# Performance work log

Measured on AMD Instinct MI355X. Metric: run time of the kernel, lower is better.

Reference implementation:

```python
import jax, jax.numpy as jnp
import numpy as np

FEAT = 512   # PLIP backbone dim
HID = 256
N_CLS_HEADS = 11   # each 3 classes -> 33 logits
N_REG_HEADS = 55   # each 1 output

def _xavier(key, shape):
    fan_in, fan_out = shape[0], shape[1]
    limit = float(np.sqrt(6.0 / (fan_in + fan_out)))
    return jax.random.uniform(key, shape, jnp.float32, -limit, limit)

def setup_inputs() -> dict:
    key = jax.random.key(0)
    ks = jax.random.split(key, 8)
    N = 200000
    x = jax.random.normal(ks[0], (1, N, FEAT), jnp.float32)
    return {
        'x': x,
        'W1': _xavier(ks[1], (FEAT, HID)), 'b1': jnp.zeros((HID,), jnp.float32),
        'Wa': _xavier(ks[2], (HID, HID)), 'ba': jnp.zeros((HID,), jnp.float32),
        'Wb': _xavier(ks[3], (HID, HID)), 'bb': jnp.zeros((HID,), jnp.float32),
        'Wc': _xavier(ks[4], (HID, 1)),  'bc': jnp.zeros((1,), jnp.float32),
        'Wr': _xavier(ks[5], (HID, HID)), 'br': jnp.zeros((HID,), jnp.float32),
        # 11 classifier heads (3 classes each) stacked into one [256, 33] GEMM
        'Wcls': _xavier(ks[6], (HID, 3 * N_CLS_HEADS)), 'bcls': jnp.zeros((3 * N_CLS_HEADS,), jnp.float32),
        'Wreg': _xavier(ks[7], (HID, N_REG_HEADS)), 'breg': jnp.zeros((N_REG_HEADS,), jnp.float32),
    }

def reference(x, W1, b1, Wa, ba, Wb, bb, Wc, bc, Wr, br, Wcls, bcls, Wreg, breg):
    xp = x[0]                                   # [N, 512]
    h = jax.nn.relu(xp @ W1 + b1)               # [N, 256]  (dropout inactive at eval)
    a = jnp.tanh(h @ Wa + ba)                   # [N, 256]
    b = jax.nn.sigmoid(h @ Wb + bb)             # [N, 256]
    A_raw = ((a * b) @ Wc + bc).T               # [1, N]
    A = jax.nn.softmax(A_raw, axis=1)           # [1, N]
    global_feat = A @ h                         # [1, 256]
    hr = jax.nn.relu(global_feat @ Wr + br)     # [1, 256]
    cls_logits = hr @ Wcls + bcls               # [1, 33] = 11 heads x 3 classes
    reg_values = (hr @ Wreg + breg)[0]          # [55]   (per-head squeeze(1))
    return A, global_feat, cls_logits, reg_values
```

## Files before the change

### kernel.cpp

```cpp
#include <hip/hip_runtime.h>
#include <stdint.h>

#define FEAT 512
#define HID  256
#define TILE 64
#define G1   768

typedef __attribute__((ext_vector_type(8))) short   short8;
typedef __attribute__((ext_vector_type(4))) float   floatx4;

__device__ inline unsigned short f2bf(float x){
  union { float f; uint32_t u; } v; v.f = x;
  uint32_t u = v.u;
  u += 0x7FFFu + ((u >> 16) & 1u);
  return (unsigned short)(u >> 16);
}
__device__ inline float bf2f(unsigned short h){
  union { uint32_t u; float f; } v; v.u = ((uint32_t)h) << 16;
  return v.f;
}
__device__ inline float sigm_f(float x){ return 1.f/(1.f + __expf(-x)); }
__device__ inline float tanh_f(float x){ return 2.f/(1.f + __expf(-2.f*x)) - 1.f; }

__global__ void prep_weights(const float* __restrict__ W1, const float* __restrict__ Wa,
                             const float* __restrict__ Wb,
                             unsigned short* __restrict__ W1bf,
                             unsigned short* __restrict__ Wabf,
                             unsigned short* __restrict__ Wbbf){
  int t = blockIdx.x*256 + threadIdx.x;
  const float* src; unsigned short* dst; int g;
  if      (t < 16384){ src = W1; dst = W1bf; g = t; }
  else if (t < 24576){ src = Wa; dst = Wabf; g = t - 16384; }
  else if (t < 32768){ src = Wb; dst = Wbbf; g = t - 24576; }
  else return;
  int lane = g & 63, nt = (g >> 6) & 15, kb = g >> 10;
  int col  = nt*16 + (lane & 15);
  int row0 = kb*32 + (lane >> 4)*8;
  unsigned short* d = dst + (size_t)g*8;
  const float*    s = src + (size_t)row0*HID + col;
  #pragma unroll
  for (int j = 0; j < 8; ++j) d[j] = f2bf(s[(size_t)j*HID]);
}

__global__ __launch_bounds__(256, 3) void fused_main(
    const float* __restrict__ x,
    const float* __restrict__ b1, const float* __restrict__ ba,
    const float* __restrict__ bb, const float* __restrict__ Wc,
    const float* __restrict__ bc,
    const unsigned short* __restrict__ W1bf,
    const unsigned short* __restrict__ Wabf,
    const unsigned short* __restrict__ Wbbf,
    float* __restrict__ s_buf, float* __restrict__ partials, int ntiles)
{
  __shared__ alignas(16) unsigned short Hs[64][264];
  __shared__ alignas(16) unsigned short Ws[8192];
  __shared__ float pbuf[4][16];

  const int tid  = threadIdx.x;
  const int wave = tid >> 6, lane = tid & 63;
  const int quad = lane >> 4, l15 = lane & 15;

  float m_run = -INFINITY, l_run = 0.f;
  float g0 = 0.f, g1 = 0.f, g2 = 0.f, g3 = 0.f;
  const float bcv = bc[0];

  for (int t = blockIdx.x; t < ntiles; t += gridDim.x){
    const int tokw = t*TILE + wave*16;

    floatx4 acc[16];
    #pragma unroll
    for (int nt = 0; nt < 16; ++nt){
      float bv = b1[nt*16 + l15];
      floatx4 tmp = {bv, bv, bv, bv};
      acc[nt] = tmp;
    }
    const float* xrow = x + (size_t)(tokw + l15)*FEAT + quad*8;
    #pragma unroll 1
    for (int kb = 0; kb < 16; ++kb){
      __syncthreads();
      { const short8* srcv = (const short8*)(W1bf + (size_t)kb*8192);
        short8* dstv = (short8*)Ws;
        #pragma unroll
        for (int c = 0; c < 4; ++c) dstv[tid + 256*c] = srcv[tid + 256*c]; }
      __syncthreads();
      const float* xp = xrow + kb*32;
      float4 xa = *(const float4*)xp;
      float4 xb = *(const float4*)(xp + 4);
      union { short8 v; unsigned short u[8]; } af;
      af.u[0]=f2bf(xa.x); af.u[1]=f2bf(xa.y); af.u[2]=f2bf(xa.z); af.u[3]=f2bf(xa.w);
      af.u[4]=f2bf(xb.x); af.u[5]=f2bf(xb.y); af.u[6]=f2bf(xb.z); af.u[7]=f2bf(xb.w);
      #pragma unroll
      for (int nt = 0; nt < 16; ++nt){
        short8 bfv = *(const short8*)&Ws[nt*512 + lane*8];
        acc[nt] = __builtin_amdgcn_mfma_f32_16x16x32_bf16(af.v, bfv, acc[nt], 0, 0, 0);
      }
    }
    #pragma unroll
    for (int nt = 0; nt < 16; ++nt){
      #pragma unroll
      for (int r = 0; r < 4; ++r){
        float hv = fmaxf(acc[nt][r], 0.f);
        Hs[wave*16 + quad*4 + r][nt*16 + l15] = f2bf(hv);
      }
    }

    float sp0 = 0.f, sp1 = 0.f, sp2 = 0.f, sp3 = 0.f;
    #pragma unroll 1
    for (int nh = 0; nh < 2; ++nh){
      floatx4 aacc[8], bacc[8];
      #pragma unroll
      for (int nt = 0; nt < 8; ++nt){
        int col = (nh*8 + nt)*16 + l15;
        float av = ba[col], bv = bb[col];
        floatx4 ta = {av, av, av, av}; aacc[nt] = ta;
        floatx4 tb = {bv, bv, bv, bv}; bacc[nt] = tb;
      }
      #pragma unroll 1
      for (int kb = 0; kb < 8; ++kb){
        __syncthreads();
        { const short8* sA = (const short8*)(Wabf + (size_t)(kb*16 + nh*8)*512);
          const short8* sB = (const short8*)(Wbbf + (size_t)(kb*16 + nh*8)*512);
          short8* dstv = (short8*)Ws;
          dstv[tid]       = sA[tid];
          dstv[tid + 256] = sA[tid + 256];
          dstv[tid + 512] = sB[tid];
          dstv[tid + 768] = sB[tid + 256]; }
        __syncthreads();
        short8 af = *(const short8*)&Hs[wave*16 + l15][kb*32 + quad*8];
        #pragma unroll
        for (int nt = 0; nt < 8; ++nt){
          short8 bA = *(const short8*)&Ws[nt*512 + lane*8];
          short8 bB = *(const short8*)&Ws[4096 + nt*512 + lane*8];
          aacc[nt] = __builtin_amdgcn_mfma_f32_16x16x32_bf16(af, bA, aacc[nt], 0, 0, 0);
          bacc[nt] = __builtin_amdgcn_mfma_f32_16x16x32_bf16(af, bB, bacc[nt], 0, 0, 0);
        }
      }
      #pragma unroll
      for (int nt = 0; nt < 8; ++nt){
        int col = (nh*8 + nt)*16 + l15;
        float wcv = Wc[col];
        sp0 += tanh_f(aacc[nt][0]) * sigm_f(bacc[nt][0]) * wcv;
        sp1 += tanh_f(aacc[nt][1]) * sigm_f(bacc[nt][1]) * wcv;
        sp2 += tanh_f(aacc[nt][2]) * sigm_f(bacc[nt][2]) * wcv;
        sp3 += tanh_f(aacc[nt][3]) * sigm_f(bacc[nt][3]) * wcv;
      }
    }
    #pragma unroll
    for (int mk = 1; mk < 16; mk <<= 1){
      sp0 += __shfl_xor(sp0, mk, 64);
      sp1 += __shfl_xor(sp1, mk, 64);
      sp2 += __shfl_xor(sp2, mk, 64);
      sp3 += __shfl_xor(sp3, mk, 64);
    }
    float s0 = sp0 + bcv, s1 = sp1 + bcv, s2 = sp2 + bcv, s3 = sp3 + bcv;
    if (l15 == 0){
      float* sb = s_buf + tokw + quad*4;
      sb[0] = s0; sb[1] = s1; sb[2] = s2; sb[3] = s3;
    }
    float tmax = fmaxf(fmaxf(s0, s1), fmaxf(s2, s3));
    tmax = fmaxf(tmax, __shfl_xor(tmax, 16, 64));
    tmax = fmaxf(tmax, __shfl_xor(tmax, 32, 64));
    float m_new = fmaxf(m_run, tmax);
    float alpha = __expf(m_run - m_new);
    float p0 = __expf(s0 - m_new), p1 = __expf(s1 - m_new);
    float p2 = __expf(s2 - m_new), p3 = __expf(s3 - m_new);
    float psum = p0 + p1 + p2 + p3;
    psum += __shfl_xor(psum, 16, 64);
    psum += __shfl_xor(psum, 32, 64);
    l_run = l_run*alpha + psum;
    m_run = m_new;
    if (l15 == 0){
      pbuf[wave][quad*4+0] = p0; pbuf[wave][quad*4+1] = p1;
      pbuf[wave][quad*4+2] = p2; pbuf[wave][quad*4+3] = p3;
    }
    g0 *= alpha; g1 *= alpha; g2 *= alpha; g3 *= alpha;
    #pragma unroll
    for (int rw = 0; rw < 16; ++rw){
      float pr = pbuf[wave][rw];
      const unsigned short* hp = &Hs[wave*16 + rw][lane*4];
      g0 += pr*bf2f(hp[0]); g1 += pr*bf2f(hp[1]);
      g2 += pr*bf2f(hp[2]); g3 += pr*bf2f(hp[3]);
    }
  }

  __syncthreads();
  float* fred = (float*)Ws;
  if (lane == 0) fred[wave] = m_run;
  __syncthreads();
  float M = fmaxf(fmaxf(fred[0], fred[1]), fmaxf(fred[2], fred[3]));
  float sc = (m_run == -INFINITY) ? 0.f : __expf(m_run - M);
  if (lane == 0) fred[4 + wave] = l_run * sc;
  fred[8 + wave*256 + lane*4 + 0] = g0*sc;
  fred[8 + wave*256 + lane*4 + 1] = g1*sc;
  fred[8 + wave*256 + lane*4 + 2] = g2*sc;
  fred[8 + wave*256 + lane*4 + 3] = g3*sc;
  __syncthreads();
  float gsum = fred[8 + 0*256 + tid] + fred[8 + 1*256 + tid]
             + fred[8 + 2*256 + tid] + fred[8 + 3*256 + tid];
  float* P = partials + (size_t)blockIdx.x*258;
  if (tid == 0){ P[0] = M; P[1] = fred[4] + fred[5] + fred[6] + fred[7]; }
  P[2 + tid] = gsum;
}

__global__ void reduce_heads(const float* __restrict__ partials,
    const float* __restrict__ Wr,   const float* __restrict__ br,
    const float* __restrict__ Wcls, const float* __restrict__ bcls,
    const float* __restrict__ Wreg, const float* __restrict__ breg,
    float* __restrict__ out, float* __restrict__ ML, int ntok)
{
  __shared__ float red[256];
  __shared__ float scw[G1];
  __shared__ float gf[256];
  __shared__ float hr[256];
  int t = threadIdx.x;

  float lm = -INFINITY;
  for (int i = t; i < G1; i += 256) lm = fmaxf(lm, partials[(size_t)i*258]);
  red[t] = lm; __syncthreads();
  for (int s = 128; s > 0; s >>= 1){ if (t < s) red[t] = fmaxf(red[t], red[t+s]); __syncthreads(); }
  float M = red[0];
  __syncthreads();

  float ll = 0.f;
  for (int i = t; i < G1; i += 256){
    float w = __expf(partials[(size_t)i*258] - M);
    scw[i] = w;
    ll += partials[(size_t)i*258 + 1] * w;
  }
  red[t] = ll; __syncthreads();
  for (int s = 128; s > 0; s >>= 1){ if (t < s) red[t] += red[t+s]; __syncthreads(); }
  float L = red[0];

  float g = 0.f;
  for (int i = 0; i < G1; ++i) g += partials[(size_t)i*258 + 2 + t] * scw[i];
  float gfv = g / L;
  gf[t] = gfv;
  out[ntok + t] = gfv;
  if (t == 0){ ML[0] = M; ML[1] = 1.f / L; }
  __syncthreads();

  float h = br[t];
  for (int c = 0; c < 256; ++c) h += gf[c] * Wr[c*256 + t];
  h = fmaxf(h, 0.f);
  hr[t] = h; __syncthreads();

  if (t < 33){
    float v = bcls[t];
    for (int j = 0; j < 256; ++j) v += hr[j] * Wcls[j*33 + t];
    out[ntok + 256 + t] = v;
  }
  if (t < 55){
    float v = breg[t];
    for (int j = 0; j < 256; ++j) v += hr[j] * Wreg[j*55 + t];
    out[ntok + 289 + t] = v;
  }
}

__global__ void finalize_A(const float* __restrict__ s_buf, const float* __restrict__ ML,
                           float* __restrict__ out, int ntok){
  int i = blockIdx.x*256 + threadIdx.x;
  if (i < ntok) out[i] = __expf(s_buf[i] - ML[0]) * ML[1];
}

extern "C" void kernel_launch(void* const* d_in, const int* in_sizes, int n_in,
                              void* d_out, int out_size, void* d_ws, size_t ws_size,
                              hipStream_t stream){
  (void)n_in; (void)out_size; (void)ws_size;
  const float* x    = (const float*)d_in[0];
  const float* W1   = (const float*)d_in[1];
  const float* b1   = (const float*)d_in[2];
  const float* Wa   = (const float*)d_in[3];
  const float* ba   = (const float*)d_in[4];
  const float* Wb   = (const float*)d_in[5];
  const float* bb   = (const float*)d_in[6];
  const float* Wc   = (const float*)d_in[7];
  const float* bc   = (const float*)d_in[8];
  const float* Wr   = (const float*)d_in[9];
  const float* br   = (const float*)d_in[10];
  const float* Wcls = (const float*)d_in[11];
  const float* bcls = (const float*)d_in[12];
  const float* Wreg = (const float*)d_in[13];
  const float* breg = (const float*)d_in[14];
  float* out = (float*)d_out;

  const int ntok   = in_sizes[0] / FEAT;
  const int ntiles = ntok / TILE;

  char* ws = (char*)d_ws;
  float* s_buf = (float*)ws;
  size_t off = (size_t)ntok * 4;
  float* partials = (float*)(ws + off); off += (size_t)G1*258*4;
  float* ML = (float*)(ws + off); off += 16;
  unsigned short* W1bf = (unsigned short*)(ws + off); off += (size_t)FEAT*HID*2;
  unsigned short* Wabf = (unsigned short*)(ws + off); off += (size_t)HID*HID*2;
  unsigned short* Wbbf = (unsigned short*)(ws + off); off += (size_t)HID*HID*2;

  prep_weights<<<128, 256, 0, stream>>>(W1, Wa, Wb, W1bf, Wabf, Wbbf);
  fused_main<<<G1, 256, 0, stream>>>(x, b1, ba, bb, Wc, bc, W1bf, Wabf, Wbbf,
                                     s_buf, partials, ntiles);
  reduce_heads<<<1, 256, 0, stream>>>(partials, Wr, br, Wcls, bcls, Wreg, breg,
                                      out, ML, ntok);
  finalize_A<<<(ntok + 255)/256, 256, 0, stream>>>(s_buf, ML, out, ntok);
}
```

Measured before the change: 750.2 us.

## Double-buffer weight tiles via direct global-to-LDS loads and prefetch activations

```diff
diff --git a/kernel.cpp b/kernel.cpp
--- a/kernel.cpp
+++ b/kernel.cpp
@@ -4,10 +4,18 @@
 #define FEAT 512
 #define HID  256
 #define TILE 64
-#define G1   768
+#define PART 512
+#define S1   64
 
 typedef __attribute__((ext_vector_type(8))) short   short8;
 typedef __attribute__((ext_vector_type(4))) float   floatx4;
+typedef unsigned int u32;
+#define AS1 __attribute__((address_space(1)))
+#define AS3 __attribute__((address_space(3)))
+
+__device__ inline void gl_lds16(const void* g, void* l){
+  __builtin_amdgcn_global_load_lds((const AS1 u32*)g, (AS3 u32*)l, 16, 0, 0);
+}
 
 __device__ inline unsigned short f2bf(float x){
   union { float f; uint32_t u; } v; v.f = x;
@@ -23,77 +31,101 @@
 __device__ inline float tanh_f(float x){ return 2.f/(1.f + __expf(-2.f*x)) - 1.f; }
 
 __global__ void prep_weights(const float* __restrict__ W1, const float* __restrict__ Wa,
-                             const float* __restrict__ Wb,
-                             unsigned short* __restrict__ W1bf,
-                             unsigned short* __restrict__ Wabf,
-                             unsigned short* __restrict__ Wbbf){
+                             const float* __restrict__ Wb, unsigned short* __restrict__ blob){
   int t = blockIdx.x*256 + threadIdx.x;
-  const float* src; unsigned short* dst; int g;
-  if      (t < 16384){ src = W1; dst = W1bf; g = t; }
-  else if (t < 24576){ src = Wa; dst = Wabf; g = t - 16384; }
-  else if (t < 32768){ src = Wb; dst = Wbbf; g = t - 24576; }
-  else return;
-  int lane = g & 63, nt = (g >> 6) & 15, kb = g >> 10;
-  int col  = nt*16 + (lane & 15);
-  int row0 = kb*32 + (lane >> 4)*8;
-  unsigned short* d = dst + (size_t)g*8;
-  const float*    s = src + (size_t)row0*HID + col;
-  #pragma unroll
-  for (int j = 0; j < 8; ++j) d[j] = f2bf(s[(size_t)j*HID]);
-}
-
-__global__ __launch_bounds__(256, 3) void fused_main(
+  if (t >= 32768) return;
+  int r = t >> 10, s = t & 1023;
+  int lane = s & 63, l15 = lane & 15, quad = lane >> 4;
+  const float* src; int col, row0;
+  if (r < 16){
+    int nt = s >> 6;
+    src = W1; col = nt*16 + l15; row0 = r*32 + quad*8;
+  } else {
+    int r2 = r - 16, nh = r2 >> 3, kb = r2 & 7;
+    int half = s >> 9, nt2 = (s >> 6) & 7;
+    src = half ? Wb : Wa;
+    col = (nh*8 + nt2)*16 + l15; row0 = kb*32 + quad*8;
+  }
+  unsigned short* d = blob + (size_t)t*8;
+  const float*   sp = src + (size_t)row0*HID + col;
+  #pragma unroll
+  for (int j = 0; j < 8; ++j) d[j] = f2bf(sp[(size_t)j*HID]);
+}
+
+__global__ __launch_bounds__(256, 2) void fused_main(
     const float* __restrict__ x,
     const float* __restrict__ b1, const float* __restrict__ ba,
     const float* __restrict__ bb, const float* __restrict__ Wc,
     const float* __restrict__ bc,
-    const unsigned short* __restrict__ W1bf,
-    const unsigned short* __restrict__ Wabf,
-    const unsigned short* __restrict__ Wbbf,
+    const unsigned short* __restrict__ blob,
     float* __restrict__ s_buf, float* __restrict__ partials, int ntiles)
 {
   __shared__ alignas(16) unsigned short Hs[64][264];
-  __shared__ alignas(16) unsigned short Ws[8192];
+  __shared__ alignas(16) unsigned short Ws[2][8192];
   __shared__ float pbuf[4][16];
 
   const int tid  = threadIdx.x;
   const int wave = tid >> 6, lane = tid & 63;
   const int quad = lane >> 4, l15 = lane & 15;
 
+  auto stage = [&](int rnd, int buf){
+    #pragma unroll
+    for (int c = 0; c < 4; ++c){
+      const unsigned short* gp = blob + (size_t)rnd*8192 + (wave*4 + c)*512 + lane*8;
+      gl_lds16((const void*)gp, (void*)&Ws[buf][(wave*4 + c)*512]);
+    }
+  };
+
+  float b1r[16], bar[16], bbr[16], wcr[16];
+  #pragma unroll
+  for (int i = 0; i < 16; ++i){
+    int ci = i*16 + l15;
+    b1r[i] = b1[ci]; bar[i] = ba[ci]; bbr[i] = bb[ci]; wcr[i] = Wc[ci];
+  }
+  const float bcv = bc[0];
+
   float m_run = -INFINITY, l_run = 0.f;
   float g0 = 0.f, g1 = 0.f, g2 = 0.f, g3 = 0.f;
-  const float bcv = bc[0];
-
+
+  float4 xa = {0,0,0,0}, xb = {0,0,0,0};
+  if (blockIdx.x < ntiles){
+    const float* xr = x + (size_t)(blockIdx.x*TILE + wave*16 + l15)*FEAT + quad*8;
+    xa = *(const float4*)xr; xb = *(const float4*)(xr + 4);
+  }
+  stage(0, 0);
+  __syncthreads();
+
+  #pragma unroll 1
   for (int t = blockIdx.x; t < ntiles; t += gridDim.x){
     const int tokw = t*TILE + wave*16;
+    const float* xrow = x + (size_t)(tokw + l15)*FEAT + quad*8;
 
     floatx4 acc[16];
     #pragma unroll
     for (int nt = 0; nt < 16; ++nt){
-      float bv = b1[nt*16 + l15];
+      float bv = b1r[nt];
       floatx4 tmp = {bv, bv, bv, bv};
       acc[nt] = tmp;
     }
-    const float* xrow = x + (size_t)(tokw + l15)*FEAT + quad*8;
-    #pragma unroll 1
+    #pragma unroll 2
     for (int kb = 0; kb < 16; ++kb){
-      __syncthreads();
-      { const short8* srcv = (const short8*)(W1bf + (size_t)kb*8192);
-        short8* dstv = (short8*)Ws;
-        #pragma unroll
-        for (int c = 0; c < 4; ++c) dstv[tid + 256*c] = srcv[tid + 256*c]; }
-      __syncthreads();
-      const float* xp = xrow + kb*32;
-      float4 xa = *(const float4*)xp;
-      float4 xb = *(const float4*)(xp + 4);
+      stage(kb + 1, (kb + 1) & 1);
+      float4 xa_n, xb_n;
+      if (kb < 15){
+        const float* xp = xrow + (kb + 1)*32;
+        xa_n = *(const float4*)xp; xb_n = *(const float4*)(xp + 4);
+      }
       union { short8 v; unsigned short u[8]; } af;
       af.u[0]=f2bf(xa.x); af.u[1]=f2bf(xa.y); af.u[2]=f2bf(xa.z); af.u[3]=f2bf(xa.w);
       af.u[4]=f2bf(xb.x); af.u[5]=f2bf(xb.y); af.u[6]=f2bf(xb.z); af.u[7]=f2bf(xb.w);
+      const unsigned short* wsb = Ws[kb & 1];
       #pragma unroll
       for (int nt = 0; nt < 16; ++nt){
-        short8 bfv = *(const short8*)&Ws[nt*512 + lane*8];
+        short8 bfv = *(const short8*)&wsb[nt*512 + lane*8];
         acc[nt] = __builtin_amdgcn_mfma_f32_16x16x32_bf16(af.v, bfv, acc[nt], 0, 0, 0);
       }
+      __syncthreads();
+      if (kb < 15){ xa = xa_n; xb = xb_n; }
     }
     #pragma unroll
     for (int nt = 0; nt < 16; ++nt){
@@ -104,45 +136,46 @@
       }
     }
 
+    {
+      int tn = t + gridDim.x;
+      if (tn < ntiles){
+        const float* xr = x + (size_t)(tn*TILE + wave*16 + l15)*FEAT + quad*8;
+        xa = *(const float4*)xr; xb = *(const float4*)(xr + 4);
+      }
+    }
+
     float sp0 = 0.f, sp1 = 0.f, sp2 = 0.f, sp3 = 0.f;
-    #pragma unroll 1
+    #pragma unroll
     for (int nh = 0; nh < 2; ++nh){
       floatx4 aacc[8], bacc[8];
       #pragma unroll
-      for (int nt = 0; nt < 8; ++nt){
-        int col = (nh*8 + nt)*16 + l15;
-        float av = ba[col], bv = bb[col];
-        floatx4 ta = {av, av, av, av}; aacc[nt] = ta;
-        floatx4 tb = {bv, bv, bv, bv}; bacc[nt] = tb;
-      }
-      #pragma unroll 1
+      for (int nt2 = 0; nt2 < 8; ++nt2){
+        float av = bar[nh*8 + nt2], bv = bbr[nh*8 + nt2];
+        floatx4 ta = {av, av, av, av}; aacc[nt2] = ta;
+        floatx4 tb = {bv, bv, bv, bv}; bacc[nt2] = tb;
+      }
+      #pragma unroll 2
       for (int kb = 0; kb < 8; ++kb){
+        const int r = nh*8 + kb;
+        stage((r == 15) ? 0 : (17 + r), (r + 1) & 1);
+        short8 af2 = *(const short8*)&Hs[wave*16 + l15][kb*32 + quad*8];
+        const unsigned short* wsb = Ws[r & 1];
+        #pragma unroll
+        for (int nt2 = 0; nt2 < 8; ++nt2){
+          short8 bA = *(const short8*)&wsb[nt2*512 + lane*8];
+          short8 bB = *(const short8*)&wsb[4096 + nt2*512 + lane*8];
+          aacc[nt2] = __builtin_amdgcn_mfma_f32_16x16x32_bf16(af2, bA, aacc[nt2], 0, 0, 0);
+          bacc[nt2] = __builtin_amdgcn_mfma_f32_16x16x32_bf16(af2, bB, bacc[nt2], 0, 0, 0);
+        }
         __syncthreads();
-        { const short8* sA = (const short8*)(Wabf + (size_t)(kb*16 + nh*8)*512);
-          const short8* sB = (const short8*)(Wbbf + (size_t)(kb*16 + nh*8)*512);
-          short8* dstv = (short8*)Ws;
-          dstv[tid]       = sA[tid];
-          dstv[tid + 256] = sA[tid + 256];
-          dstv[tid + 512] = sB[tid];
-          dstv[tid + 768] = sB[tid + 256]; }
-        __syncthreads();
-        short8 af = *(const short8*)&Hs[wave*16 + l15][kb*32 + quad*8];
-        #pragma unroll
-        for (int nt = 0; nt < 8; ++nt){
-          short8 bA = *(const short8*)&Ws[nt*512 + lane*8];
-          short8 bB = *(const short8*)&Ws[4096 + nt*512 + lane*8];
-          aacc[nt] = __builtin_amdgcn_mfma_f32_16x16x32_bf16(af, bA, aacc[nt], 0, 0, 0);
-          bacc[nt] = __builtin_amdgcn_mfma_f32_16x16x32_bf16(af, bB, bacc[nt], 0, 0, 0);
-        }
       }
       #pragma unroll
-      for (int nt = 0; nt < 8; ++nt){
-        int col = (nh*8 + nt)*16 + l15;
-        float wcv = Wc[col];
-        sp0 += tanh_f(aacc[nt][0]) * sigm_f(bacc[nt][0]) * wcv;
-        sp1 += tanh_f(aacc[nt][1]) * sigm_f(bacc[nt][1]) * wcv;
-        sp2 += tanh_f(aacc[nt][2]) * sigm_f(bacc[nt][2]) * wcv;
-        sp3 += tanh_f(aacc[nt][3]) * sigm_f(bacc[nt][3]) * wcv;
+      for (int nt2 = 0; nt2 < 8; ++nt2){
+        float wcv = wcr[nh*8 + nt2];
+        sp0 += tanh_f(aacc[nt2][0]) * sigm_f(bacc[nt2][0]) * wcv;
+        sp1 += tanh_f(aacc[nt2][1]) * sigm_f(bacc[nt2][1]) * wcv;
+        sp2 += tanh_f(aacc[nt2][2]) * sigm_f(bacc[nt2][2]) * wcv;
+        sp3 += tanh_f(aacc[nt2][3]) * sigm_f(bacc[nt2][3]) * wcv;
       }
     }
     #pragma unroll
@@ -184,7 +217,7 @@
   }
 
   __syncthreads();
-  float* fred = (float*)Ws;
+  float* fred = (float*)(&Ws[0][0]);
   if (lane == 0) fred[wave] = m_run;
   __syncthreads();
   float M = fmaxf(fmaxf(fred[0], fred[1]), fmaxf(fred[2], fred[3]));
@@ -202,37 +235,58 @@
   P[2 + tid] = gsum;
 }
 
-__global__ void reduce_heads(const float* __restrict__ partials,
+__global__ void reduce_stage1(const float* __restrict__ partials, float* __restrict__ p2){
+  int j = blockIdx.x, t = threadIdx.x;
+  const float* base = partials + (size_t)j*8*258;
+  float m = -INFINITY;
+  #pragma unroll
+  for (int k = 0; k < 8; ++k) m = fmaxf(m, base[k*258]);
+  float w[8]; float l = 0.f;
+  #pragma unroll
+  for (int k = 0; k < 8; ++k){
+    w[k] = __expf(base[k*258] - m);
+    l += base[k*258 + 1] * w[k];
+  }
+  float g = 0.f;
+  #pragma unroll
+  for (int k = 0; k < 8; ++k) g += base[k*258 + 2 + t] * w[k];
+  float* o = p2 + (size_t)j*258;
+  if (t == 0){ o[0] = m; o[1] = l; }
+  o[2 + t] = g;
+}
+
+__global__ void reduce_heads(const float* __restrict__ p2,
     const float* __restrict__ Wr,   const float* __restrict__ br,
     const float* __restrict__ Wcls, const float* __restrict__ bcls,
     const float* __restrict__ Wreg, const float* __restrict__ breg,
     float* __restrict__ out, float* __restrict__ ML, int ntok)
 {
   __shared__ float red[256];
-  __shared__ float scw[G1];
+  __shared__ float scw[S1];
   __shared__ float gf[256];
   __shared__ float hr[256];
   int t = threadIdx.x;
 
-  float lm = -INFINITY;
-  for (int i = t; i < G1; i += 256) lm = fmaxf(lm, partials[(size_t)i*258]);
+  float lm = (t < S1) ? p2[(size_t)t*258] : -INFINITY;
   red[t] = lm; __syncthreads();
   for (int s = 128; s > 0; s >>= 1){ if (t < s) red[t] = fmaxf(red[t], red[t+s]); __syncthreads(); }
   float M = red[0];
   __syncthreads();
 
   float ll = 0.f;
-  for (int i = t; i < G1; i += 256){
-    float w = __expf(partials[(size_t)i*258] - M);
-    scw[i] = w;
-    ll += partials[(size_t)i*258 + 1] * w;
+  if (t < S1){
+    float w = __expf(p2[(size_t)t*258] - M);
+    scw[t] = w;
+    ll = p2[(size_t)t*258 + 1] * w;
   }
   red[t] = ll; __syncthreads();
   for (int s = 128; s > 0; s >>= 1){ if (t < s) red[t] += red[t+s]; __syncthreads(); }
   float L = red[0];
+  __syncthreads();
 
   float g = 0.f;
-  for (int i = 0; i < G1; ++i) g += partials[(size_t)i*258 + 2 + t] * scw[i];
+  #pragma unroll 16
+  for (int i = 0; i < S1; ++i) g += p2[(size_t)i*258 + 2 + t] * scw[i];
   float gfv = g / L;
   gf[t] = gfv;
   out[ntok + t] = gfv;
@@ -240,26 +294,36 @@
   __syncthreads();
 
   float h = br[t];
+  #pragma unroll 8
   for (int c = 0; c < 256; ++c) h += gf[c] * Wr[c*256 + t];
   h = fmaxf(h, 0.f);
   hr[t] = h; __syncthreads();
 
   if (t < 33){
     float v = bcls[t];
+    #pragma unroll 8
     for (int j = 0; j < 256; ++j) v += hr[j] * Wcls[j*33 + t];
     out[ntok + 256 + t] = v;
   }
   if (t < 55){
     float v = breg[t];
+    #pragma unroll 8
     for (int j = 0; j < 256; ++j) v += hr[j] * Wreg[j*55 + t];
     out[ntok + 289 + t] = v;
   }
 }
 
 __global__ void finalize_A(const float* __restrict__ s_buf, const float* __restrict__ ML,
-                           float* __restrict__ out, int ntok){
+                           float* __restrict__ out, int n4){
   int i = blockIdx.x*256 + threadIdx.x;
-  if (i < ntok) out[i] = __expf(s_buf[i] - ML[0]) * ML[1];
+  if (i < n4){
+    float M = ML[0], Li = ML[1];
+    float4 s = ((const float4*)s_buf)[i];
+    float4 o;
+    o.x = __expf(s.x - M)*Li; o.y = __expf(s.y - M)*Li;
+    o.z = __expf(s.z - M)*Li; o.w = __expf(s.w - M)*Li;
+    ((float4*)out)[i] = o;
+  }
 }
 
 extern "C" void kernel_launch(void* const* d_in, const int* in_sizes, int n_in,
@@ -289,16 +353,16 @@
   char* ws = (char*)d_ws;
   float* s_buf = (float*)ws;
   size_t off = (size_t)ntok * 4;
-  float* partials = (float*)(ws + off); off += (size_t)G1*258*4;
-  float* ML = (float*)(ws + off); off += 16;
-  unsigned short* W1bf = (unsigned short*)(ws + off); off += (size_t)FEAT*HID*2;
-  unsigned short* Wabf = (unsigned short*)(ws + off); off += (size_t)HID*HID*2;
-  unsigned short* Wbbf = (unsigned short*)(ws + off); off += (size_t)HID*HID*2;
-
-  prep_weights<<<128, 256, 0, stream>>>(W1, Wa, Wb, W1bf, Wabf, Wbbf);
-  fused_main<<<G1, 256, 0, stream>>>(x, b1, ba, bb, Wc, bc, W1bf, Wabf, Wbbf,
-                                     s_buf, partials, ntiles);
-  reduce_heads<<<1, 256, 0, stream>>>(partials, Wr, br, Wcls, bcls, Wreg, breg,
+  float* partials = (float*)(ws + off); off += (size_t)PART*258*4;
+  float* p2       = (float*)(ws + off); off += (size_t)S1*258*4;
+  float* ML       = (float*)(ws + off); off += 16;
+  unsigned short* blob = (unsigned short*)(ws + off); off += 32*8192*2;
+
+  prep_weights<<<128, 256, 0, stream>>>(W1, Wa, Wb, blob);
+  fused_main<<<PART, 256, 0, stream>>>(x, b1, ba, bb, Wc, bc, blob,
+                                       s_buf, partials, ntiles);
+  reduce_stage1<<<S1, 256, 0, stream>>>(partials, p2);
+  reduce_heads<<<1, 256, 0, stream>>>(p2, Wr, br, Wcls, bcls, Wreg, breg,
                                       out, ML, ntok);
-  finalize_A<<<(ntok + 255)/256, 256, 0, stream>>>(s_buf, ML, out, ntok);
-}
+  finalize_A<<<(ntok/4 + 255)/256, 256, 0, stream>>>(s_buf, ML, out, ntok/4);
+}
```

Measured after the change: 757.4 us. Within noise of the previous version (+1.0%).
